# Kernel tuning notes

Hardware: AMD Instinct MI355X
Metric: run time of the kernel (lower is better)

Reference implementation:

```python
import jax, jax.numpy as jnp
import numpy as np

N_NODES = 100000
N_EDGES = 1600000
IN_F, HID_F, OUT_F = 64, 64, 64


def setup_inputs() -> dict:
    key = jax.random.key(0)
    ks = jax.random.split(key, 9)
    return {
        "x": jax.random.normal(ks[0], (N_NODES, IN_F), dtype=jnp.float32),
        "src": jax.random.randint(ks[1], (N_EDGES,), 0, N_NODES, dtype=jnp.int64),
        "dst": jax.random.randint(ks[2], (N_EDGES,), 0, N_NODES, dtype=jnp.int64),
        "W_self1": jax.random.normal(ks[3], (IN_F, HID_F), dtype=jnp.float32) * (1.0 / np.sqrt(IN_F)),
        "W_neigh1": jax.random.normal(ks[4], (IN_F, HID_F), dtype=jnp.float32) * (1.0 / np.sqrt(IN_F)),
        "b1": jnp.zeros((HID_F,), dtype=jnp.float32),
        "W_self2": jax.random.normal(ks[5], (HID_F, OUT_F), dtype=jnp.float32) * (1.0 / np.sqrt(HID_F)),
        "W_neigh2": jax.random.normal(ks[6], (HID_F, OUT_F), dtype=jnp.float32) * (1.0 / np.sqrt(HID_F)),
        "b2": jnp.zeros((OUT_F,), dtype=jnp.float32),
    }


def reference(x, src, dst, W_self1, W_neigh1, b1, W_self2, W_neigh2, b2):
    N = x.shape[0]
    # in-degree per destination node; zero-in-degree nodes get zero aggregate (DGL semantics)
    deg = jax.ops.segment_sum(jnp.ones(dst.shape, dtype=x.dtype), dst, num_segments=N)
    inv_deg = jnp.where(deg > 0, 1.0 / jnp.maximum(deg, 1.0), 0.0)[:, None]  # [N,1]

    def sage_conv(h, W_s, W_n, b):
        # mean over in-neighbors: gather src feats, segment-sum at dst, normalize
        agg = jax.ops.segment_sum(h[src], dst, num_segments=N) * inv_deg  # [N,F]
        return h @ W_s + agg @ W_n + b

    h = jax.nn.relu(sage_conv(x, W_self1, W_neigh1, b1))
    return sage_conv(h, W_self2, W_neigh2, b2)
```

## Files before the change

### kernel.cpp

```cpp
#include <hip/hip_runtime.h>

#define N_NODES 100000
#define N_EDGES 1600000
#define NBKT 196
#define BKT_SHIFT 9
#define BKT_MASK 511
#define NT_TILES 6250

typedef __attribute__((ext_vector_type(8))) short short8;
typedef __attribute__((ext_vector_type(4))) float float4v;

__device__ __forceinline__ unsigned short f2bf(float f) {
  unsigned u = __float_as_uint(f);
  return (unsigned short)((u + 0x7fffu + ((u >> 16) & 1u)) >> 16);
}
__device__ __forceinline__ float bflo(unsigned d) { return __uint_as_float(d << 16); }
__device__ __forceinline__ float bfhi(unsigned d) { return __uint_as_float(d & 0xffff0000u); }


__global__ void kA_count(const int* __restrict__ dst, int* __restrict__ blkCnt) {
  __shared__ int hist[NBKT];
  for (int t = threadIdx.x; t < NBKT; t += 256) hist[t] = 0;
  __syncthreads();
  const int chunk = (N_EDGES + gridDim.x - 1) / gridDim.x;
  const int e0 = blockIdx.x * chunk;
  const int e1 = min(e0 + chunk, N_EDGES);
  for (int e = e0 + threadIdx.x; e < e1; e += 256)
    atomicAdd(&hist[dst[e] >> BKT_SHIFT], 1);
  __syncthreads();
  for (int t = threadIdx.x; t < NBKT; t += 256)
    blkCnt[t * 256 + blockIdx.x] = hist[t];
}

__global__ void kA_scan1(int* __restrict__ blkCnt, int* __restrict__ bktTot) {
  const int b = blockIdx.x;
  const int tid = threadIdx.x, lane = tid & 63, w = tid >> 6;
  int v = blkCnt[b * 256 + tid];
  int inc = v;
  #pragma unroll
  for (int d = 1; d < 64; d <<= 1) { int y = __shfl_up(inc, d); if (lane >= d) inc += y; }
  __shared__ int wtot[4];
  if (lane == 63) wtot[w] = inc;
  __syncthreads();
  int base = 0;
  for (int j = 0; j < w; j++) base += wtot[j];
  blkCnt[b * 256 + tid] = base + inc - v;
  if (tid == 255) bktTot[b] = base + inc;
}

__global__ void kA_scan2(const int* __restrict__ bktTot, int* __restrict__ bktStart) {
  int lane = threadIdx.x;
  int running = 0;
  for (int base = 0; base < NBKT; base += 64) {
    int i = base + lane;
    int v = (i < NBKT) ? bktTot[i] : 0;
    int inc = v;
    #pragma unroll
    for (int d = 1; d < 64; d <<= 1) { int y = __shfl_up(inc, d); if (lane >= d) inc += y; }
    if (i < NBKT) bktStart[i] = running + inc - v;
    running += __shfl(inc, 63);
  }
}

__global__ void kA_scatter(const int* __restrict__ src, const int* __restrict__ dst,
                           const int* __restrict__ blkCnt, const int* __restrict__ bktStart,
                           int* __restrict__ binned) {
  __shared__ int curb[NBKT];
  for (int t = threadIdx.x; t < NBKT; t += 256)
    curb[t] = bktStart[t] + blkCnt[t * 256 + blockIdx.x];
  __syncthreads();
  const int chunk = (N_EDGES + gridDim.x - 1) / gridDim.x;
  const int e0 = blockIdx.x * chunk;
  const int e1 = min(e0 + chunk, N_EDGES);
  for (int e = e0 + threadIdx.x; e < e1; e += 256) {
    int d = dst[e];
    int s = src[e];
    int b = d >> BKT_SHIFT;
    int p = atomicAdd(&curb[b], 1);
    binned[p] = s | ((d & BKT_MASK) << 17);
  }
}


__global__ void k_sort(const int* __restrict__ binned, const int* __restrict__ bktStart,
                       const int* __restrict__ bktTot,
                       int* __restrict__ off, int* __restrict__ esrc) {
  const int b = blockIdx.x;
  const int tid = threadIdx.x, lane = tid & 63, w = tid >> 6;
  __shared__ int cnt[512];
  __shared__ int pos[512];
  cnt[tid] = 0; cnt[tid + 256] = 0;
  __syncthreads();
  const int s0 = bktStart[b], ne = bktTot[b];
  for (int i = tid; i < ne; i += 256)
    atomicAdd(&cnt[binned[s0 + i] >> 17], 1);
  __syncthreads();
  int c0 = cnt[2 * tid], c1 = cnt[2 * tid + 1];
  int v = c0 + c1;
  int inc = v;
  #pragma unroll
  for (int d = 1; d < 64; d <<= 1) { int y = __shfl_up(inc, d); if (lane >= d) inc += y; }
  __shared__ int wtot[4];
  if (lane == 63) wtot[w] = inc;
  __syncthreads();
  int base = s0;
  for (int j = 0; j < w; j++) base += wtot[j];
  int ex = base + inc - v;
  pos[2 * tid] = ex;
  pos[2 * tid + 1] = ex + c0;
  int n0 = (b << BKT_SHIFT) + 2 * tid;
  if (n0 < N_NODES)     off[n0] = ex;
  if (n0 + 1 < N_NODES) off[n0 + 1] = ex + c0;
  if (b == NBKT - 1 && tid == 0) off[N_NODES] = N_EDGES;
  __syncthreads();
  for (int i = tid; i < ne; i += 256) {
    int pe = binned[s0 + i];
    int p = atomicAdd(&pos[pe >> 17], 1);
    esrc[p] = pe & 0x1FFFF;
  }
}


__global__ void k_prep(const float* __restrict__ in, unsigned short* __restrict__ outb,
                       const float* __restrict__ W0, const float* __restrict__ W1,
                       const float* __restrict__ W2, const float* __restrict__ W3,
                       unsigned short* __restrict__ F) {
  if (blockIdx.x < NT_TILES) {
    int i = blockIdx.x * 256 + threadIdx.x;
    float4 v = ((const float4*)in)[i];
    unsigned d0 = ((unsigned)f2bf(v.y) << 16) | f2bf(v.x);
    unsigned d1 = ((unsigned)f2bf(v.w) << 16) | f2bf(v.z);
    ((uint2*)outb)[i] = make_uint2(d0, d1);
    return;
  }
  if (threadIdx.x >= 64) return;
  const int wsel = blockIdx.x - NT_TILES;
  const float* W = (wsel == 0) ? W0 : (wsel == 1) ? W1 : (wsel == 2) ? W2 : W3;
  unsigned short* out = F + wsel * 4096;
  int lane = threadIdx.x;
  int col = lane & 15, kr = lane >> 4;
  #pragma unroll
  for (int kc = 0; kc < 2; kc++)
    #pragma unroll
    for (int nt = 0; nt < 4; nt++) {
      unsigned d[4];
      #pragma unroll
      for (int jj = 0; jj < 4; jj++) {
        float w0 = W[(kc * 32 + kr * 8 + 2 * jj)     * 64 + nt * 16 + col];
        float w1 = W[(kc * 32 + kr * 8 + 2 * jj + 1) * 64 + nt * 16 + col];
        d[jj] = ((unsigned)f2bf(w1) << 16) | f2bf(w0);
      }
      uint4* p = (uint4*)(out + ((kc * 4 + nt) * 64 + lane) * 8);
      *p = make_uint4(d[0], d[1], d[2], d[3]);
    }
}


template <bool RELU, bool OUT_BF>
__global__ void k_fused(const unsigned short* __restrict__ featb,
                        const int* __restrict__ off, const int* __restrict__ esrc,
                        const unsigned short* __restrict__ wfS,
                        const unsigned short* __restrict__ wfN,
                        const float* __restrict__ bias,
                        float* __restrict__ outf, unsigned short* __restrict__ outb) {
  __shared__ unsigned short aggl[4][16 * 64];
  const int tid = threadIdx.x;
  const int lane = tid & 63;
  const int wslot = tid >> 6;
  const int t = (blockIdx.x * blockDim.x + tid) >> 6;
  if (t >= NT_TILES) return;

  unsigned short* lw = &aggl[wslot][0];
  const int r = lane >> 3;
  const int c = lane & 7;

  int o1 = off[t * 16];
  for (int j = 0; j < 16; ++j) {
    const int o0 = o1;
    o1 = off[t * 16 + j + 1];
    float acc[8];
    #pragma unroll
    for (int q = 0; q < 8; q++) acc[q] = 0.f;

    int i = o0;
    for (; i + 16 <= o1; i += 16) {
      int sA = esrc[i + r];
      int sB = esrc[i + 8 + r];
      uint4 vA = *(const uint4*)(featb + sA * 64 + c * 8);
      uint4 vB = *(const uint4*)(featb + sB * 64 + c * 8);
      acc[0] += bflo(vA.x); acc[1] += bfhi(vA.x);
      acc[2] += bflo(vA.y); acc[3] += bfhi(vA.y);
      acc[4] += bflo(vA.z); acc[5] += bfhi(vA.z);
      acc[6] += bflo(vA.w); acc[7] += bfhi(vA.w);
      acc[0] += bflo(vB.x); acc[1] += bfhi(vB.x);
      acc[2] += bflo(vB.y); acc[3] += bfhi(vB.y);
      acc[4] += bflo(vB.z); acc[5] += bfhi(vB.z);
      acc[6] += bflo(vB.w); acc[7] += bfhi(vB.w);
    }
    if (i + 8 <= o1) {
      int s = esrc[i + r];
      uint4 v = *(const uint4*)(featb + s * 64 + c * 8);
      acc[0] += bflo(v.x); acc[1] += bfhi(v.x);
      acc[2] += bflo(v.y); acc[3] += bfhi(v.y);
      acc[4] += bflo(v.z); acc[5] += bfhi(v.z);
      acc[6] += bflo(v.w); acc[7] += bfhi(v.w);
      i += 8;
    }
    if (i < o1) {
      int e = i + r;
      if (e < o1) {
        int s = esrc[e];
        uint4 v = *(const uint4*)(featb + s * 64 + c * 8);
        acc[0] += bflo(v.x); acc[1] += bfhi(v.x);
        acc[2] += bflo(v.y); acc[3] += bfhi(v.y);
        acc[4] += bflo(v.z); acc[5] += bfhi(v.z);
        acc[6] += bflo(v.w); acc[7] += bfhi(v.w);
      }
    }
    #pragma unroll
    for (int m = 8; m <= 32; m <<= 1)
      #pragma unroll
      for (int q = 0; q < 8; q++) acc[q] += __shfl_xor(acc[q], m);

    const int dg = o1 - o0;
    const float inv = (dg > 0) ? (1.0f / (float)dg) : 0.f;
    if (r == 0) {
      unsigned d0 = ((unsigned)f2bf(acc[1] * inv) << 16) | f2bf(acc[0] * inv);
      unsigned d1 = ((unsigned)f2bf(acc[3] * inv) << 16) | f2bf(acc[2] * inv);
      unsigned d2 = ((unsigned)f2bf(acc[5] * inv) << 16) | f2bf(acc[4] * inv);
      unsigned d3 = ((unsigned)f2bf(acc[7] * inv) << 16) | f2bf(acc[6] * inv);
      *(uint4*)(lw + j * 64 + ((c ^ (j & 7)) << 3)) = make_uint4(d0, d1, d2, d3);
    }
  }

  __builtin_amdgcn_wave_barrier();
  asm volatile("" ::: "memory");

  const int col = lane & 15, rr = lane >> 4;
  const int m = t * 16 + col;
  short8 as0 = *(const short8*)(featb + m * 64 + rr * 8);
  short8 as1 = *(const short8*)(featb + m * 64 + 32 + rr * 8);
  short8 aa0 = *(const short8*)(lw + col * 64 + ((rr ^ (col & 7)) << 3));
  short8 aa1 = *(const short8*)(lw + col * 64 + (((rr + 4) ^ (col & 7)) << 3));

  #pragma unroll
  for (int nt = 0; nt < 4; nt++) {
    short8 bs0 = *(const short8*)(wfS + ((0 * 4 + nt) * 64 + lane) * 8);
    short8 bs1 = *(const short8*)(wfS + ((1 * 4 + nt) * 64 + lane) * 8);
    short8 bn0 = *(const short8*)(wfN + ((0 * 4 + nt) * 64 + lane) * 8);
    short8 bn1 = *(const short8*)(wfN + ((1 * 4 + nt) * 64 + lane) * 8);
    float bvn = bias[nt * 16 + col];
    float4v cfr = {bvn, bvn, bvn, bvn};
    cfr = __builtin_amdgcn_mfma_f32_16x16x32_bf16(as0, bs0, cfr, 0, 0, 0);
    cfr = __builtin_amdgcn_mfma_f32_16x16x32_bf16(as1, bs1, cfr, 0, 0, 0);
    cfr = __builtin_amdgcn_mfma_f32_16x16x32_bf16(aa0, bn0, cfr, 0, 0, 0);
    cfr = __builtin_amdgcn_mfma_f32_16x16x32_bf16(aa1, bn1, cfr, 0, 0, 0);
    #pragma unroll
    for (int r2 = 0; r2 < 4; r2++) {
      int row = t * 16 + rr * 4 + r2;
      float v = cfr[r2];
      if (RELU) v = fmaxf(v, 0.f);
      if (OUT_BF) outb[row * 64 + nt * 16 + col] = f2bf(v);
      else        outf[row * 64 + nt * 16 + col] = v;
    }
  }
}


extern "C" void kernel_launch(void* const* d_in, const int* in_sizes, int n_in,
                              void* d_out, int out_size, void* d_ws, size_t ws_size,
                              hipStream_t stream) {
  const float* x   = (const float*)d_in[0];
  const int*   src = (const int*)d_in[1];
  const int*   dst = (const int*)d_in[2];
  const float* Ws1 = (const float*)d_in[3];
  const float* Wn1 = (const float*)d_in[4];
  const float* b1  = (const float*)d_in[5];
  const float* Ws2 = (const float*)d_in[6];
  const float* Wn2 = (const float*)d_in[7];
  const float* b2  = (const float*)d_in[8];

  char* ws = (char*)d_ws;
  int*            blkCnt   = (int*)(ws + 0);
  int*            bktTot   = (int*)(ws + 262144);
  int*            bktStart = (int*)(ws + 266240);
  unsigned short* wf       = (unsigned short*)(ws + 270336);
  int*            binned   = (int*)(ws + 303104);
  int*            off      = (int*)(ws + 6703104);
  int*            esrc     = (int*)(ws + 7103488);
  unsigned short* xbf      = (unsigned short*)(ws + 13503488);
  unsigned short* hbf      = (unsigned short*)(ws + 26303488);

  kA_count<<<256, 256, 0, stream>>>(dst, blkCnt);
  kA_scan1<<<NBKT, 256, 0, stream>>>(blkCnt, bktTot);
  kA_scan2<<<1, 64, 0, stream>>>(bktTot, bktStart);
  kA_scatter<<<256, 256, 0, stream>>>(src, dst, blkCnt, bktStart, binned);
  k_sort<<<NBKT, 256, 0, stream>>>(binned, bktStart, bktTot, off, esrc);

  k_prep<<<NT_TILES + 4, 256, 0, stream>>>(x, xbf, Ws1, Wn1, Ws2, Wn2, wf);

  k_fused<true, true><<<1563, 256, 0, stream>>>(xbf, off, esrc, wf + 0 * 4096,
                                                wf + 1 * 4096, b1, nullptr, hbf);
  k_fused<false, false><<<1563, 256, 0, stream>>>(hbf, off, esrc, wf + 2 * 4096,
                                                  wf + 3 * 4096, b2, (float*)d_out, nullptr);
}
```

Baseline: 238.6 us.

## Fuse prep with count, fold bucket scan into consumers, gather one node per lane group

```diff
diff --git a/kernel.cpp b/kernel.cpp
--- a/kernel.cpp
+++ b/kernel.cpp
@@ -6,6 +6,7 @@
 #define BKT_SHIFT 9
 #define BKT_MASK 511
 #define NT_TILES 6250
+#define CNT_BLOCKS 256
 
 typedef __attribute__((ext_vector_type(8))) short short8;
 typedef __attribute__((ext_vector_type(4))) float float4v;
@@ -17,19 +18,69 @@
 __device__ __forceinline__ float bflo(unsigned d) { return __uint_as_float(d << 16); }
 __device__ __forceinline__ float bfhi(unsigned d) { return __uint_as_float(d & 0xffff0000u); }
 
-
-__global__ void kA_count(const int* __restrict__ dst, int* __restrict__ blkCnt) {
+__device__ __forceinline__ void acc_add(float a[8], uint4 v) {
+  a[0] += bflo(v.x); a[1] += bfhi(v.x);
+  a[2] += bflo(v.y); a[3] += bfhi(v.y);
+  a[4] += bflo(v.z); a[5] += bfhi(v.z);
+  a[6] += bflo(v.w); a[7] += bfhi(v.w);
+}
+__device__ __forceinline__ void acc_fma(float a[8], uint4 v, float m) {
+  a[0] = fmaf(m, bflo(v.x), a[0]); a[1] = fmaf(m, bfhi(v.x), a[1]);
+  a[2] = fmaf(m, bflo(v.y), a[2]); a[3] = fmaf(m, bfhi(v.y), a[3]);
+  a[4] = fmaf(m, bflo(v.z), a[4]); a[5] = fmaf(m, bfhi(v.z), a[5]);
+  a[6] = fmaf(m, bflo(v.w), a[6]); a[7] = fmaf(m, bfhi(v.w), a[7]);
+}
+
+
+__global__ void k_prep_count(const float* __restrict__ in, unsigned short* __restrict__ outb,
+                             const float* __restrict__ W0, const float* __restrict__ W1,
+                             const float* __restrict__ W2, const float* __restrict__ W3,
+                             unsigned short* __restrict__ F,
+                             const int* __restrict__ dst, int* __restrict__ blkCnt) {
   __shared__ int hist[NBKT];
+  const int bid = blockIdx.x;
+  if (bid < NT_TILES) {
+    int i = bid * 256 + threadIdx.x;
+    float4 v = ((const float4*)in)[i];
+    unsigned d0 = ((unsigned)f2bf(v.y) << 16) | f2bf(v.x);
+    unsigned d1 = ((unsigned)f2bf(v.w) << 16) | f2bf(v.z);
+    ((uint2*)outb)[i] = make_uint2(d0, d1);
+    return;
+  }
+  if (bid < NT_TILES + 4) {
+    if (threadIdx.x >= 64) return;
+    const int wsel = bid - NT_TILES;
+    const float* W = (wsel == 0) ? W0 : (wsel == 1) ? W1 : (wsel == 2) ? W2 : W3;
+    unsigned short* out = F + wsel * 4096;
+    int lane = threadIdx.x;
+    int col = lane & 15, kr = lane >> 4;
+    #pragma unroll
+    for (int kc = 0; kc < 2; kc++)
+      #pragma unroll
+      for (int nt = 0; nt < 4; nt++) {
+        unsigned d[4];
+        #pragma unroll
+        for (int jj = 0; jj < 4; jj++) {
+          float w0 = W[(kc * 32 + kr * 8 + 2 * jj)     * 64 + nt * 16 + col];
+          float w1 = W[(kc * 32 + kr * 8 + 2 * jj + 1) * 64 + nt * 16 + col];
+          d[jj] = ((unsigned)f2bf(w1) << 16) | f2bf(w0);
+        }
+        uint4* p = (uint4*)(out + ((kc * 4 + nt) * 64 + lane) * 8);
+        *p = make_uint4(d[0], d[1], d[2], d[3]);
+      }
+    return;
+  }
+  const int cb = bid - NT_TILES - 4;
   for (int t = threadIdx.x; t < NBKT; t += 256) hist[t] = 0;
   __syncthreads();
-  const int chunk = (N_EDGES + gridDim.x - 1) / gridDim.x;
-  const int e0 = blockIdx.x * chunk;
-  const int e1 = min(e0 + chunk, N_EDGES);
+  const int chunk = N_EDGES / CNT_BLOCKS;
+  const int e0 = cb * chunk;
+  const int e1 = e0 + chunk;
   for (int e = e0 + threadIdx.x; e < e1; e += 256)
     atomicAdd(&hist[dst[e] >> BKT_SHIFT], 1);
   __syncthreads();
   for (int t = threadIdx.x; t < NBKT; t += 256)
-    blkCnt[t * 256 + blockIdx.x] = hist[t];
+    blkCnt[t * 256 + cb] = hist[t];
 }
 
 __global__ void kA_scan1(int* __restrict__ blkCnt, int* __restrict__ bktTot) {
@@ -48,31 +99,32 @@
   if (tid == 255) bktTot[b] = base + inc;
 }
 
-__global__ void kA_scan2(const int* __restrict__ bktTot, int* __restrict__ bktStart) {
-  int lane = threadIdx.x;
-  int running = 0;
-  for (int base = 0; base < NBKT; base += 64) {
-    int i = base + lane;
-    int v = (i < NBKT) ? bktTot[i] : 0;
-    int inc = v;
-    #pragma unroll
-    for (int d = 1; d < 64; d <<= 1) { int y = __shfl_up(inc, d); if (lane >= d) inc += y; }
-    if (i < NBKT) bktStart[i] = running + inc - v;
-    running += __shfl(inc, 63);
-  }
-}
-
 __global__ void kA_scatter(const int* __restrict__ src, const int* __restrict__ dst,
-                           const int* __restrict__ blkCnt, const int* __restrict__ bktStart,
+                           const int* __restrict__ blkCnt, const int* __restrict__ bktTot,
                            int* __restrict__ binned) {
+  __shared__ int bs[NBKT];
   __shared__ int curb[NBKT];
-  for (int t = threadIdx.x; t < NBKT; t += 256)
-    curb[t] = bktStart[t] + blkCnt[t * 256 + blockIdx.x];
-  __syncthreads();
-  const int chunk = (N_EDGES + gridDim.x - 1) / gridDim.x;
+  const int tid = threadIdx.x;
+  if (tid < 64) {
+    int running = 0;
+    for (int base = 0; base < NBKT; base += 64) {
+      int i = base + tid;
+      int v = (i < NBKT) ? bktTot[i] : 0;
+      int inc = v;
+      #pragma unroll
+      for (int d = 1; d < 64; d <<= 1) { int y = __shfl_up(inc, d); if (tid >= d) inc += y; }
+      if (i < NBKT) bs[i] = running + inc - v;
+      running += __shfl(inc, 63);
+    }
+  }
+  __syncthreads();
+  for (int t = tid; t < NBKT; t += 256)
+    curb[t] = bs[t] + blkCnt[t * 256 + blockIdx.x];
+  __syncthreads();
+  const int chunk = N_EDGES / CNT_BLOCKS;
   const int e0 = blockIdx.x * chunk;
-  const int e1 = min(e0 + chunk, N_EDGES);
-  for (int e = e0 + threadIdx.x; e < e1; e += 256) {
+  const int e1 = e0 + chunk;
+  for (int e = e0 + tid; e < e1; e += 256) {
     int d = dst[e];
     int s = src[e];
     int b = d >> BKT_SHIFT;
@@ -82,77 +134,46 @@
 }
 
 
-__global__ void k_sort(const int* __restrict__ binned, const int* __restrict__ bktStart,
-                       const int* __restrict__ bktTot,
+__global__ void k_sort(const int* __restrict__ binned, const int* __restrict__ bktTot,
                        int* __restrict__ off, int* __restrict__ esrc) {
   const int b = blockIdx.x;
   const int tid = threadIdx.x, lane = tid & 63, w = tid >> 6;
   __shared__ int cnt[512];
   __shared__ int pos[512];
-  cnt[tid] = 0; cnt[tid + 256] = 0;
-  __syncthreads();
-  const int s0 = bktStart[b], ne = bktTot[b];
-  for (int i = tid; i < ne; i += 256)
+  __shared__ int wtot[8];
+  __shared__ int s0sh;
+  cnt[tid] = 0;
+  if (tid < 64) {
+    int sum = 0;
+    for (int i = tid; i < b; i += 64) sum += bktTot[i];
+    #pragma unroll
+    for (int m = 1; m < 64; m <<= 1) sum += __shfl_xor(sum, m);
+    if (tid == 0) s0sh = sum;
+  }
+  __syncthreads();
+  const int s0 = s0sh, ne = bktTot[b];
+  for (int i = tid; i < ne; i += 512)
     atomicAdd(&cnt[binned[s0 + i] >> 17], 1);
   __syncthreads();
-  int c0 = cnt[2 * tid], c1 = cnt[2 * tid + 1];
-  int v = c0 + c1;
-  int inc = v;
+  int c = cnt[tid];
+  int inc = c;
   #pragma unroll
   for (int d = 1; d < 64; d <<= 1) { int y = __shfl_up(inc, d); if (lane >= d) inc += y; }
-  __shared__ int wtot[4];
   if (lane == 63) wtot[w] = inc;
   __syncthreads();
   int base = s0;
   for (int j = 0; j < w; j++) base += wtot[j];
-  int ex = base + inc - v;
-  pos[2 * tid] = ex;
-  pos[2 * tid + 1] = ex + c0;
-  int n0 = (b << BKT_SHIFT) + 2 * tid;
-  if (n0 < N_NODES)     off[n0] = ex;
-  if (n0 + 1 < N_NODES) off[n0 + 1] = ex + c0;
+  int ex = base + inc - c;
+  pos[tid] = ex;
+  int n0 = (b << BKT_SHIFT) + tid;
+  if (n0 < N_NODES) off[n0] = ex;
   if (b == NBKT - 1 && tid == 0) off[N_NODES] = N_EDGES;
   __syncthreads();
-  for (int i = tid; i < ne; i += 256) {
+  for (int i = tid; i < ne; i += 512) {
     int pe = binned[s0 + i];
     int p = atomicAdd(&pos[pe >> 17], 1);
     esrc[p] = pe & 0x1FFFF;
   }
-}
-
-
-__global__ void k_prep(const float* __restrict__ in, unsigned short* __restrict__ outb,
-                       const float* __restrict__ W0, const float* __restrict__ W1,
-                       const float* __restrict__ W2, const float* __restrict__ W3,
-                       unsigned short* __restrict__ F) {
-  if (blockIdx.x < NT_TILES) {
-    int i = blockIdx.x * 256 + threadIdx.x;
-    float4 v = ((const float4*)in)[i];
-    unsigned d0 = ((unsigned)f2bf(v.y) << 16) | f2bf(v.x);
-    unsigned d1 = ((unsigned)f2bf(v.w) << 16) | f2bf(v.z);
-    ((uint2*)outb)[i] = make_uint2(d0, d1);
-    return;
-  }
-  if (threadIdx.x >= 64) return;
-  const int wsel = blockIdx.x - NT_TILES;
-  const float* W = (wsel == 0) ? W0 : (wsel == 1) ? W1 : (wsel == 2) ? W2 : W3;
-  unsigned short* out = F + wsel * 4096;
-  int lane = threadIdx.x;
-  int col = lane & 15, kr = lane >> 4;
-  #pragma unroll
-  for (int kc = 0; kc < 2; kc++)
-    #pragma unroll
-    for (int nt = 0; nt < 4; nt++) {
-      unsigned d[4];
-      #pragma unroll
-      for (int jj = 0; jj < 4; jj++) {
-        float w0 = W[(kc * 32 + kr * 8 + 2 * jj)     * 64 + nt * 16 + col];
-        float w1 = W[(kc * 32 + kr * 8 + 2 * jj + 1) * 64 + nt * 16 + col];
-        d[jj] = ((unsigned)f2bf(w1) << 16) | f2bf(w0);
-      }
-      uint4* p = (uint4*)(out + ((kc * 4 + nt) * 64 + lane) * 8);
-      *p = make_uint4(d[0], d[1], d[2], d[3]);
-    }
 }
 
 
@@ -171,66 +192,47 @@
   if (t >= NT_TILES) return;
 
   unsigned short* lw = &aggl[wslot][0];
-  const int r = lane >> 3;
-  const int c = lane & 7;
-
-  int o1 = off[t * 16];
-  for (int j = 0; j < 16; ++j) {
-    const int o0 = o1;
-    o1 = off[t * 16 + j + 1];
-    float acc[8];
+  const int n = lane >> 3;
+  const int h = lane & 7;
+
+  #pragma unroll
+  for (int half = 0; half < 2; ++half) {
+    const int row = half * 8 + n;
+    const int node = t * 16 + row;
+    const int o0 = off[node];
+    const int o1 = off[node + 1];
+    float a[8];
     #pragma unroll
-    for (int q = 0; q < 8; q++) acc[q] = 0.f;
+    for (int q = 0; q < 8; q++) a[q] = 0.f;
 
     int i = o0;
-    for (; i + 16 <= o1; i += 16) {
-      int sA = esrc[i + r];
-      int sB = esrc[i + 8 + r];
-      uint4 vA = *(const uint4*)(featb + sA * 64 + c * 8);
-      uint4 vB = *(const uint4*)(featb + sB * 64 + c * 8);
-      acc[0] += bflo(vA.x); acc[1] += bfhi(vA.x);
-      acc[2] += bflo(vA.y); acc[3] += bfhi(vA.y);
-      acc[4] += bflo(vA.z); acc[5] += bfhi(vA.z);
-      acc[6] += bflo(vA.w); acc[7] += bfhi(vA.w);
-      acc[0] += bflo(vB.x); acc[1] += bfhi(vB.x);
-      acc[2] += bflo(vB.y); acc[3] += bfhi(vB.y);
-      acc[4] += bflo(vB.z); acc[5] += bfhi(vB.z);
-      acc[6] += bflo(vB.w); acc[7] += bfhi(vB.w);
-    }
-    if (i + 8 <= o1) {
-      int s = esrc[i + r];
-      uint4 v = *(const uint4*)(featb + s * 64 + c * 8);
-      acc[0] += bflo(v.x); acc[1] += bfhi(v.x);
-      acc[2] += bflo(v.y); acc[3] += bfhi(v.y);
-      acc[4] += bflo(v.z); acc[5] += bfhi(v.z);
-      acc[6] += bflo(v.w); acc[7] += bfhi(v.w);
-      i += 8;
+    for (; i + 4 <= o1; i += 4) {
+      int s0 = esrc[i], s1 = esrc[i + 1], s2 = esrc[i + 2], s3 = esrc[i + 3];
+      uint4 v0 = *(const uint4*)(featb + s0 * 64 + h * 8);
+      uint4 v1 = *(const uint4*)(featb + s1 * 64 + h * 8);
+      uint4 v2 = *(const uint4*)(featb + s2 * 64 + h * 8);
+      uint4 v3 = *(const uint4*)(featb + s3 * 64 + h * 8);
+      acc_add(a, v0); acc_add(a, v1); acc_add(a, v2); acc_add(a, v3);
     }
     if (i < o1) {
-      int e = i + r;
-      if (e < o1) {
-        int s = esrc[e];
-        uint4 v = *(const uint4*)(featb + s * 64 + c * 8);
-        acc[0] += bflo(v.x); acc[1] += bfhi(v.x);
-        acc[2] += bflo(v.y); acc[3] += bfhi(v.y);
-        acc[4] += bflo(v.z); acc[5] += bfhi(v.z);
-        acc[6] += bflo(v.w); acc[7] += bfhi(v.w);
-      }
+      int last = o1 - 1;
+      int e1 = min(i + 1, last), e2 = min(i + 2, last);
+      float m1 = (i + 1 < o1) ? 1.f : 0.f;
+      float m2 = (i + 2 < o1) ? 1.f : 0.f;
+      int s0 = esrc[i], s1 = esrc[e1], s2 = esrc[e2];
+      uint4 v0 = *(const uint4*)(featb + s0 * 64 + h * 8);
+      uint4 v1 = *(const uint4*)(featb + s1 * 64 + h * 8);
+      uint4 v2 = *(const uint4*)(featb + s2 * 64 + h * 8);
+      acc_add(a, v0); acc_fma(a, v1, m1); acc_fma(a, v2, m2);
     }
-    #pragma unroll
-    for (int m = 8; m <= 32; m <<= 1)
-      #pragma unroll
-      for (int q = 0; q < 8; q++) acc[q] += __shfl_xor(acc[q], m);
 
     const int dg = o1 - o0;
     const float inv = (dg > 0) ? (1.0f / (float)dg) : 0.f;
-    if (r == 0) {
-      unsigned d0 = ((unsigned)f2bf(acc[1] * inv) << 16) | f2bf(acc[0] * inv);
-      unsigned d1 = ((unsigned)f2bf(acc[3] * inv) << 16) | f2bf(acc[2] * inv);
-      unsigned d2 = ((unsigned)f2bf(acc[5] * inv) << 16) | f2bf(acc[4] * inv);
-      unsigned d3 = ((unsigned)f2bf(acc[7] * inv) << 16) | f2bf(acc[6] * inv);
-      *(uint4*)(lw + j * 64 + ((c ^ (j & 7)) << 3)) = make_uint4(d0, d1, d2, d3);
-    }
+    unsigned d0 = ((unsigned)f2bf(a[1] * inv) << 16) | f2bf(a[0] * inv);
+    unsigned d1 = ((unsigned)f2bf(a[3] * inv) << 16) | f2bf(a[2] * inv);
+    unsigned d2 = ((unsigned)f2bf(a[5] * inv) << 16) | f2bf(a[4] * inv);
+    unsigned d3 = ((unsigned)f2bf(a[7] * inv) << 16) | f2bf(a[6] * inv);
+    *(uint4*)(lw + row * 64 + ((h ^ (row & 7)) << 3)) = make_uint4(d0, d1, d2, d3);
   }
 
   __builtin_amdgcn_wave_barrier();
@@ -283,7 +285,6 @@
   char* ws = (char*)d_ws;
   int*            blkCnt   = (int*)(ws + 0);
   int*            bktTot   = (int*)(ws + 262144);
-  int*            bktStart = (int*)(ws + 266240);
   unsigned short* wf       = (unsigned short*)(ws + 270336);
   int*            binned   = (int*)(ws + 303104);
   int*            off      = (int*)(ws + 6703104);
@@ -291,13 +292,11 @@
   unsigned short* xbf      = (unsigned short*)(ws + 13503488);
   unsigned short* hbf      = (unsigned short*)(ws + 26303488);
 
-  kA_count<<<256, 256, 0, stream>>>(dst, blkCnt);
+  k_prep_count<<<NT_TILES + 4 + CNT_BLOCKS, 256, 0, stream>>>(
+      x, xbf, Ws1, Wn1, Ws2, Wn2, wf, dst, blkCnt);
   kA_scan1<<<NBKT, 256, 0, stream>>>(blkCnt, bktTot);
-  kA_scan2<<<1, 64, 0, stream>>>(bktTot, bktStart);
-  kA_scatter<<<256, 256, 0, stream>>>(src, dst, blkCnt, bktStart, binned);
-  k_sort<<<NBKT, 256, 0, stream>>>(binned, bktStart, bktTot, off, esrc);
-
-  k_prep<<<NT_TILES + 4, 256, 0, stream>>>(x, xbf, Ws1, Wn1, Ws2, Wn2, wf);
+  kA_scatter<<<CNT_BLOCKS, 256, 0, stream>>>(src, dst, blkCnt, bktTot, binned);
+  k_sort<<<NBKT, 512, 0, stream>>>(binned, bktTot, off, esrc);
 
   k_fused<true, true><<<1563, 256, 0, stream>>>(xbf, off, esrc, wf + 0 * 4096,
                                                 wf + 1 * 4096, b1, nullptr, hbf);
```

After: 199.7 us. 1.19x faster.
